# Performance work log

Hardware: AMD Instinct MI355X
Metric: run time of the kernel (lower is better)

## Reference

```python
import jax, jax.numpy as jnp
import numpy as np

T = 1048576      # signal length
K = 3            # number of IMFs
ALPHA = 2000.0   # bandwidth penalty
TAU = 1e-7       # dual ascent step
TOL = 1e-6       # convergence tolerance
N_ITER = 50      # max fixed-point iterations


def _vmd(x, omega_init):
    T_ = x.shape[0]
    t = jnp.arange(1, T_ + 1, dtype=jnp.float32) / T_
    freqs = t - 0.5 - 1.0 / T_                           # [T]
    f_hat = jnp.fft.fftshift(jnp.fft.fft(x))             # [T] complex
    u0 = jnp.zeros((K, T_), dtype=f_hat.dtype)
    lam0 = jnp.zeros((T_,), dtype=f_hat.dtype)

    def step(carry, n):
        u_prev, lam_prev, omega, done = carry
        base = (freqs[None, :] - omega[:, None]) ** 2    # [K,T]
        # mode k's denom also gets (freqs-omega[k-1])^2 and (freqs-omega[k+1])^2
        nbr = jnp.zeros_like(base).at[1:].add(base[:-1]).at[:-1].add(base[1:])
        denom = base + nbr + TAU ** 2
        u_hat = (f_hat[None, :] - lam_prev[None, :] / 2.0) / (1.0 + ALPHA * denom)
        pw = jnp.real(u_hat) ** 2 + jnp.imag(u_hat) ** 2  # |u_hat|^2, [K,T]
        omega_new = jnp.sum(freqs[None, :] * pw, axis=1) / jnp.sum(pw, axis=1)
        lam_new = lam_prev + TAU * (jnp.sum(u_hat, axis=0) - f_hat)
        # convergence check (every 10th iter), mirrors the original break
        u_diff = jnp.sum(jnp.abs(u_hat - u_prev) ** 2) / jnp.sum(jnp.abs(u_prev) ** 2)
        om_diff = jnp.sum(jnp.abs(omega_new - jnp.roll(omega_new, 1))) / K
        conv = (n % 10 == 0) & (u_diff < TOL) & (om_diff < TOL)
        # freeze state once converged (break-iteration's fresh u_hat is kept)
        u_out = jnp.where(done, u_prev, u_hat)
        lam_out = jnp.where(done, lam_prev, lam_new)
        om_out = jnp.where(done, omega, omega_new)
        return (u_out, lam_out, om_out, done | conv), None

    init = (u0, lam0, omega_init.astype(jnp.float32), jnp.array(False))
    (u_hat, _, _, _), _ = jax.lax.scan(jax.checkpoint(step), init, jnp.arange(N_ITER))
    imfs = jnp.real(jnp.fft.ifft(jnp.fft.ifftshift(u_hat, axes=-1), axis=-1))
    return imfs.astype(jnp.float32)                      # [K,T]


def setup_inputs() -> dict:
    key = jax.random.key(0)
    kx, ko = jax.random.split(key)
    x = jax.random.normal(kx, (T,), dtype=jnp.float32)
    omega_init = jax.random.uniform(ko, (K,), dtype=jnp.float32) * 0.5  # init==1
    return {"x": x, "omega_init": omega_init}


def reference(x, omega_init):
    return _vmd(x, omega_init)
```

## Files before the change

### kernel.cpp

```cpp
#include <hip/hip_runtime.h>
#include <math.h>


#define ALPHA_F 2000.0f
#define TAU_F   1e-7f

static __device__ __forceinline__ int lpad2(int i) { return i + (i >> 4); }
static __device__ __forceinline__ int swz(int i)  { return ((i & 7) << 7) | (i >> 3); }
static __device__ __forceinline__ int swzA(int i) { return ((i & 7) << 6) | (i >> 3); }
static __device__ __forceinline__ float frcp(float x) { return __builtin_amdgcn_rcpf(x); }

typedef float v2f __attribute__((ext_vector_type(2)));
static __device__ __forceinline__ v2f sp(float s) { v2f r; r.x = s; r.y = s; return r; }
static __device__ __forceinline__ v2f v2(float a, float b) { v2f r; r.x = a; r.y = b; return r; }
static __device__ __forceinline__ v2f pkfma(v2f a, v2f b, v2f c)
{ return __builtin_elementwise_fma(a, b, c); }
static __device__ __forceinline__ v2f cmul(v2f a, v2f w)
{
  v2f t = a * sp(w.x);
  v2f s = v2(-a.y, a.x);
  return pkfma(s, sp(w.y), t);
}
static __device__ __forceinline__ v2f cmulrr(v2f a, float wr, float wi)
{
  v2f t = a * sp(wr);
  v2f s = v2(-a.y, a.x);
  return pkfma(s, sp(wi), t);
}

#define PADN2 1088

template<int CTRL>
static __device__ __forceinline__ float dpp_addf(float v)
{
  int r = __builtin_amdgcn_update_dpp(0, __float_as_int(v), CTRL, 0xf, 0xf, true);
  return v + __int_as_float(r);
}
static __device__ __forceinline__ float wave64_sum(float v)
{
  v = dpp_addf<0x111>(v);
  v = dpp_addf<0x112>(v);
  v = dpp_addf<0x114>(v);
  v = dpp_addf<0x118>(v);
  v = dpp_addf<0x142>(v);
  v = dpp_addf<0x143>(v);
  return v;
}
static __device__ __forceinline__ float row16_sum(float v)
{
  v = dpp_addf<0x111>(v);
  v = dpp_addf<0x112>(v);
  v = dpp_addf<0x114>(v);
  v = dpp_addf<0x118>(v);
  return v;
}
static __device__ __forceinline__ float rdlane(float v, int l)
{
  return __int_as_float(__builtin_amdgcn_readlane(__float_as_int(v), l));
}

template<int SIGN>
static __device__ void fft1024p_reg(v2f X0, v2f X1, v2f X2, v2f X3,
                                    v2f* A, v2f* B)
{
  const int u = threadIdx.x;
  {
    v2f t0 = X0 + X2, t1 = X0 - X2, t2 = X1 + X3, t3 = X1 - X3;
    v2f o0 = t0 + t2, o2 = t0 - t2;
    v2f ns3 = v2(t3.y, -t3.x);
    v2f o1, o3;
    if (SIGN < 0) { o1 = t1 + ns3; o3 = t1 - ns3; }
    else          { o1 = t1 - ns3; o3 = t1 + ns3; }
    const int base = u << 2;
    B[lpad2(base    )] = o0; B[lpad2(base + 1)] = o1;
    B[lpad2(base + 2)] = o2; B[lpad2(base + 3)] = o3;
    __syncthreads();
  }
#pragma unroll
  for (int st = 1; st < 5; ++st) {
    v2f *in  = (st & 1) ? B : A;
    v2f *out = (st & 1) ? A : B;
    const int quarter = 1 << (2 * st);
    const int p = u & (quarter - 1);
    const int g = u >> (2 * st);

    float sw, cw;
    sincospif((float)(2 * p) * (1.0f / (float)(4 << (2 * st))), &sw, &cw);
    const float w1r = cw, w1i = (SIGN < 0) ? -sw : sw;
    const float w2r = w1r * w1r - w1i * w1i, w2i = 2.0f * w1r * w1i;
    const float w3r = w2r * w1r - w2i * w1i, w3i = w2r * w1i + w2i * w1r;

    v2f Y0 = in[lpad2(u)], Y1 = in[lpad2(u + 256)];
    v2f Y2 = in[lpad2(u + 512)], Y3 = in[lpad2(u + 768)];

    v2f y1 = cmulrr(Y1, w1r, w1i), y2 = cmulrr(Y2, w2r, w2i),
        y3 = cmulrr(Y3, w3r, w3i);

    v2f t0 = Y0 + y2, t1 = Y0 - y2, t2 = y1 + y3, t3 = y1 - y3;
    v2f o0 = t0 + t2, o2 = t0 - t2;
    v2f ns3 = v2(t3.y, -t3.x);
    v2f o1, o3;
    if (SIGN < 0) { o1 = t1 + ns3; o3 = t1 - ns3; }
    else          { o1 = t1 - ns3; o3 = t1 + ns3; }

    const int base = (g << (2 * st + 2)) + p;
    out[lpad2(base              )] = o0;
    out[lpad2(base +     quarter)] = o1;
    out[lpad2(base + 2 * quarter)] = o2;
    out[lpad2(base + 3 * quarter)] = o3;
    __syncthreads();
  }
}

__global__ __launch_bounds__(256) void k_fwd_passA(const float* __restrict__ x,
                                                   float2* __restrict__ ws0)
{
  __shared__ __align__(16) v2f A[PADN2], B[PADN2];
  const int p = swzA(blockIdx.x);
  const int tid = threadIdx.x;
  const int c0 = 2 * p;
  v2f X[4];
#pragma unroll
  for (int q = 0; q < 4; ++q)
    X[q] = ((const v2f*)x)[(size_t)(tid + 256 * q) * 512 + p];
  fft1024p_reg<-1>(X[0], X[1], X[2], X[3], A, B);

  float sa, ca, sb, cb, ssa, cca, ssb, ccb;
  sincospif((float)(c0 * tid) * (2.0f / 1048576.0f), &sa, &ca);
  sincospif((float)((c0 + 1) * tid) * (2.0f / 1048576.0f), &sb, &cb);
  sincospif((float)c0 * (1.0f / 2048.0f), &ssa, &cca);
  sincospif((float)(c0 + 1) * (1.0f / 2048.0f), &ssb, &ccb);
  v2f E0 = v2(ca, -sa), E1 = v2(cb, -sb);
  const v2f S0 = v2(cca, -ssa), S1 = v2(ccb, -ssb);
#pragma unroll
  for (int q = 0; q < 4; ++q) {
    int k = tid + 256 * q;
    int kk = (1024 - k) & 1023;
    v2f Z = B[lpad2(k)];
    v2f Wv = B[lpad2(kk)];
    float X0r = 0.5f * (Z.x + Wv.x), X0i = 0.5f * (Z.y - Wv.y);
    float X1r = 0.5f * (Z.y + Wv.y), X1i = 0.5f * (Wv.x - Z.x);
    v2f o01 = cmul(v2(X0r, X0i), E0);
    v2f o23 = cmul(v2(X1r, X1i), E1);
    float4 o = make_float4(o01.x, o01.y, o23.x, o23.y);
    ((float4*)ws0)[(size_t)k * 512 + p] = o;
    E0 = cmul(E0, S0); E1 = cmul(E1, S1);
  }
}

__global__ __launch_bounds__(256) void k_fwd_passB(const float2* __restrict__ ws0,
                                                   float2* __restrict__ fhat,
                                                   float* __restrict__ ET)
{
  __shared__ __align__(16) v2f A[PADN2], B[PADN2];
  const int b = swz(blockIdx.x);
  const int tid = threadIdx.x;
  v2f X[4];
#pragma unroll
  for (int q = 0; q < 4; ++q)
    X[q] = ((const v2f*)ws0)[(size_t)b * 1024 + tid + 256 * q];
  fft1024p_reg<-1>(X[0], X[1], X[2], X[3], A, B);
#pragma unroll
  for (int q = 0; q < 4; ++q) {
    int k2 = tid + 256 * q;
    v2f v = B[lpad2(k2)];
    fhat[(size_t)b * 1024 + k2] = make_float2(v.x, v.y);
    ET[(size_t)k2 * 1024 + b] = v.x * v.x + v.y * v.y;
  }
}

static __device__ __forceinline__ void lag4(float x, float& l0, float& l1,
                                            float& l2, float& l3)
{
  float m0 = x, m1 = x - (1.0f / 3.0f), m2 = x - (2.0f / 3.0f), m3 = x - 1.0f;
  l0 = -4.5f * m1 * m2 * m3;
  l1 = 13.5f * m0 * m2 * m3;
  l2 = -13.5f * m0 * m1 * m3;
  l3 =  4.5f * m0 * m1 * m2;
}

__global__ __launch_bounds__(256) void k_moments(const float* __restrict__ ET,
                                                 double* __restrict__ W)
{
  __shared__ double red[4 * 4];
  const int B = blockIdx.x;
  const int k2 = B ^ 512;
  const int tid = threadIdx.x;
  double a0 = 0, a1 = 0, a2 = 0, a3 = 0;
#pragma unroll
  for (int q = 0; q < 4; ++q) {
    int k1 = tid + 256 * q;
    float e = ET[(size_t)k2 * 1024 + k1];
    float l0, l1, l2, l3;
    lag4((float)k1 * (1.0f / 1024.0f), l0, l1, l2, l3);
    a0 += (double)(e * l0); a1 += (double)(e * l1);
    a2 += (double)(e * l2); a3 += (double)(e * l3);
  }
  const int lane = tid & 63, wv = tid >> 6;
  double pv[4] = { a0, a1, a2, a3 };
#pragma unroll
  for (int j = 0; j < 4; ++j) {
    double v = pv[j];
    for (int off = 32; off; off >>= 1) v += __shfl_down(v, off, 64);
    if (lane == 0) red[wv * 4 + j] = v;
  }
  __syncthreads();
  if (tid < 4)
    W[B * 4 + tid] = red[tid] + red[4 + tid] + red[8 + tid] + red[12 + tid];
}

__global__ __launch_bounds__(1024) void k_solve(
    const double* __restrict__ W4, const float* __restrict__ omega_init,
    float* __restrict__ ckeepN, float* __restrict__ omegaF)
{
  __shared__ float red[2][6 * 16];
  const int t = threadIdx.x;
  const int lane = t & 63, wv = t >> 6;

  float Wsc[4], fsc[4];
#pragma unroll
  for (int e = 0; e < 4; ++e) {
    Wsc[e] = (float)W4[t * 4 + e];
    fsc[e] = (float)((double)t / 1024.0 + (double)e / 3072.0 - 0.5);
  }
  const v2f frP = v2(fsc[0], fsc[1]), frQ = v2(fsc[2], fsc[3]);
  const v2f WrP = v2(Wsc[0], Wsc[1]), WrQ = v2(Wsc[2], Wsc[3]);
  const v2f WfP = WrP * frP,          WfQ = WrQ * frQ;
  v2f cnrP = sp(0.0f), cnrQ = sp(0.0f);

  float om0 = omega_init[0], om1 = omega_init[1], om2 = omega_init[2];

#pragma unroll 1
  for (int it = 0; it < 49; ++it) {
    float* rb = red[it & 1];
    v2f p0 = sp(0.f), p1 = sp(0.f), p2 = sp(0.f),
        p3 = sp(0.f), p4 = sp(0.f), p5 = sp(0.f);

    auto node_pair = [&](const v2f fv, const v2f Wrv, const v2f Wfv, v2f& cnv) {
      v2f a0 = fv - sp(om0), a1 = fv - sp(om1), a2 = fv - sp(om2);
      v2f d0 = a0 * a0, d1 = a1 * a1, d2 = a2 * a2;
      v2f s01 = d0 + d1, s12 = d1 + d2;
      v2f dA = pkfma(sp(ALPHA_F), s01, sp(1.0f));
      v2f dC = pkfma(sp(ALPHA_F), s12, sp(1.0f));
      v2f dB = pkfma(sp(ALPHA_F), d2, dA);
      v2f AB = dA * dB, BC = dB * dC, AC = dA * dC;
      v2f ABC = AB * dC;
      v2f r = v2(frcp(ABC.x), frcp(ABC.y));
      v2f w0 = BC * r, w1 = AC * r, w2 = AB * r;
      v2f hf = pkfma(sp(-0.5f), cnv, sp(1.0f));
      v2f g = hf * hf;
      v2f gw0 = g * (w0 * w0), gw1 = g * (w1 * w1), gw2 = g * (w2 * w2);
      p0 = pkfma(Wfv, gw0, p0); p1 = pkfma(Wfv, gw1, p1); p2 = pkfma(Wfv, gw2, p2);
      p3 = pkfma(Wrv, gw0, p3); p4 = pkfma(Wrv, gw1, p4); p5 = pkfma(Wrv, gw2, p5);
      v2f S = (w0 + w1) + w2;
      cnv = pkfma(sp(TAU_F), pkfma(S, hf, sp(-1.0f)), cnv);
    };
    node_pair(frP, WrP, WfP, cnrP);
    node_pair(frQ, WrQ, WfQ, cnrQ);

    float q0 = p0.x + p0.y, q1 = p1.x + p1.y, q2 = p2.x + p2.y;
    float q3 = p3.x + p3.y, q4 = p4.x + p4.y, q5 = p5.x + p5.y;

    q0 = wave64_sum(q0); q1 = wave64_sum(q1); q2 = wave64_sum(q2);
    q3 = wave64_sum(q3); q4 = wave64_sum(q4); q5 = wave64_sum(q5);
    if (lane == 63) {
      rb[0 * 16 + wv] = q0; rb[1 * 16 + wv] = q1; rb[2 * 16 + wv] = q2;
      rb[3 * 16 + wv] = q3; rb[4 * 16 + wv] = q4; rb[5 * 16 + wv] = q5;
    }
    __syncthreads();
    float v1 = rb[lane];
    float v2_ = rb[64 + (lane & 31)];
    v1 = row16_sum(v1);
    v2_ = row16_sum(v2_);
    float n0 = rdlane(v1, 15), n1 = rdlane(v1, 31), n2 = rdlane(v1, 47);
    float e0 = rdlane(v1, 63), e1 = rdlane(v2_, 15), e2 = rdlane(v2_, 31);
    om0 = n0 * frcp(e0);
    om1 = n1 * frcp(e1);
    om2 = n2 * frcp(e2);
  }

  ((float4*)ckeepN)[t] = make_float4(cnrP.x, cnrP.y, cnrQ.x, cnrQ.y);
  if (t == 0) { omegaF[0] = om0; omegaF[1] = om1; omegaF[2] = om2; }
}

__global__ __launch_bounds__(256) void k_inv_A2(
    const float2* __restrict__ fhat, const float* __restrict__ ckeepN,
    const float* __restrict__ omegaF, float2* __restrict__ ws0)
{
  __shared__ __align__(16) v2f A[PADN2], B[PADN2];
  __shared__ float cn4[4096];
  __shared__ float som[3];
  const int tid = threadIdx.x;
  const int b = swz(blockIdx.x);
  for (int i = tid; i < 1024; i += 256)
    ((float4*)cn4)[i] = ((const float4*)ckeepN)[i];
  if (tid == 0) { som[0] = omegaF[0]; som[1] = omegaF[1]; som[2] = omegaF[2]; }
  __syncthreads();
  const float om0 = som[0], om1 = som[1], om2 = som[2];
  const float xb = (float)b * (1.0f / 1024.0f);
  float l0, l1, l2, l3, m0, m1, m2, m3;
  lag4(xb, l0, l1, l2, l3);
  lag4(1.0f - xb, m0, m1, m2, m3);

  v2f X[4];
  v2f v2reg[4];
#pragma unroll
  for (int q = 0; q < 4; ++q) {
    int j = tid + 256 * q;
    float2 f = fhat[(size_t)b * 1024 + j];
    int bin = j ^ 512;
    int binp = 1023 - bin;
    float4 cv = ((const float4*)cn4)[bin];
    float4 cw = ((const float4*)cn4)[binp];
    float c  = l0 * cv.x + l1 * cv.y + l2 * cv.z + l3 * cv.w;
    float cp = m0 * cw.x + m1 * cw.y + m2 * cw.z + m3 * cw.w;
    float hf = 1.0f - 0.5f * c;
    float hp = 1.0f - 0.5f * cp;
    int tt = (bin << 10) | b;
    float freq = (float)tt * (1.0f / 1048576.0f) - 0.5f;
    v2f fpm = v2(freq, -freq);
    v2f A0 = fpm - sp(om0), A1 = fpm - sp(om1), A2v = fpm - sp(om2);
    v2f D0 = A0 * A0, D1 = A1 * A1, D2 = A2v * A2v;
    v2f DA = pkfma(sp(ALPHA_F), D0 + D1, sp(1.0f));
    v2f DB = pkfma(sp(ALPHA_F), D2, DA);
    float r0 = hf * frcp(DA.x), r0n = hp * frcp(DA.y);
    float r1 = hf * frcp(DB.x), r1n = hp * frcp(DB.y);
    float Rr = 0.5f * (r0 + r0n), Ri = 0.5f * (r1 + r1n);
    X[q] = cmul(v2(f.x, f.y), v2(Rr, Ri));
    v2f DC = pkfma(sp(ALPHA_F), D1 + D2, sp(1.0f));
    float r2 = hf * frcp(DC.x), r2n = hp * frcp(DC.y);
    float Rr2 = 0.5f * (r2 + r2n);
    v2reg[q] = v2(f.x, f.y) * sp(Rr2);
  }
  fft1024p_reg<1>(X[0], X[1], X[2], X[3], A, B);

  float sa, ca, ss, cs;
  sincospif((float)(b * tid) * (2.0f / 1048576.0f), &sa, &ca);
  sincospif((float)b * (1.0f / 2048.0f), &ss, &cs);
  const v2f Einit = v2(ca, sa);
  const v2f S = v2(cs, ss);

  v2f E = Einit;
#pragma unroll
  for (int q = 0; q < 4; ++q) {
    int m1i = tid + 256 * q;
    v2f v = B[lpad2(m1i)];
    v2f o = cmul(v, E);
    ws0[(size_t)m1i * 1024 + b] = make_float2(o.x, o.y);
    E = cmul(E, S);
  }
  __syncthreads();
  fft1024p_reg<1>(v2reg[0], v2reg[1], v2reg[2], v2reg[3], A, B);

  E = Einit;
#pragma unroll
  for (int q = 0; q < 4; ++q) {
    int m1i = tid + 256 * q;
    v2f v = B[lpad2(m1i)];
    v2f o = cmul(v, E);
    ws0[1048576 + (size_t)m1i * 1024 + b] = make_float2(o.x, o.y);
    E = cmul(E, S);
  }
}

__global__ __launch_bounds__(256) void k_inv_B2(const float2* __restrict__ ws0,
                                                float* __restrict__ out)
{
  __shared__ __align__(16) v2f A[PADN2], B[PADN2];
  const int tid = threadIdx.x;
  const float sc = 1.0f / 1048576.0f;

  if (blockIdx.x < 1024) {
    const int b = swz(blockIdx.x);
    v2f X[4];
#pragma unroll
    for (int q = 0; q < 4; ++q)
      X[q] = ((const v2f*)ws0)[(size_t)b * 1024 + tid + 256 * q];
    fft1024p_reg<1>(X[0], X[1], X[2], X[3], A, B);
#pragma unroll
    for (int q = 0; q < 4; ++q) {
      int m2 = tid + 256 * q;
      v2f v = B[lpad2(m2)];
      out[(size_t)m2 * 1024 + b]           = v.x * sc;
      out[1048576 + (size_t)m2 * 1024 + b] = v.y * sc;
    }
  } else {
    const int s = swzA(blockIdx.x - 1024);
    const int b0 = 2 * s, b1 = 2 * s + 1;
#pragma unroll
    for (int q = 0; q < 4; ++q) {
      int j = tid + 256 * q;
      A[lpad2(j)] = ((const v2f*)ws0)[1048576 + (size_t)b0 * 1024 + j];
      B[lpad2(j)] = ((const v2f*)ws0)[1048576 + (size_t)b1 * 1024 + j];
    }
    __syncthreads();
    v2f Z[4];
#pragma unroll
    for (int q = 0; q < 4; ++q) {
      int j = tid + 256 * q;
      int mj = (1024 - j) & 1023;
      v2f W0j = A[lpad2(j)], W0m = A[lpad2(mj)];
      v2f W1j = B[lpad2(j)], W1m = B[lpad2(mj)];
      float H0r = 0.5f * (W0j.x + W0m.x), H0i = 0.5f * (W0j.y - W0m.y);
      float H1r = 0.5f * (W1j.x + W1m.x), H1i = 0.5f * (W1j.y - W1m.y);
      Z[q] = v2(H0r - H1i, H0i + H1r);
    }
    __syncthreads();
    fft1024p_reg<1>(Z[0], Z[1], Z[2], Z[3], A, B);
#pragma unroll
    for (int q = 0; q < 4; ++q) {
      int m2 = tid + 256 * q;
      v2f v = B[lpad2(m2)];
      out[2097152 + (size_t)m2 * 1024 + b0] = v.x * sc;
      out[2097152 + (size_t)m2 * 1024 + b1] = v.y * sc;
    }
  }
}

extern "C" void kernel_launch(void* const* d_in, const int* in_sizes, int n_in,
                              void* d_out, int out_size, void* d_ws, size_t ws_size,
                              hipStream_t stream)
{
  (void)in_sizes; (void)n_in; (void)out_size; (void)ws_size;
  const float* x       = (const float*)d_in[0];
  const float* om_init = (const float*)d_in[1];
  float* out = (float*)d_out;

  char* w = (char*)d_ws;
  const size_t MB = 1024ull * 1024ull;
  float2* fhat     = (float2*)(w);
  float*  ET       = (float*)(w + 8 * MB);
  double* W4       = (double*)(w + 12 * MB);
  float*  ckeepN   = (float*)(w + 12 * MB + 32 * 1024);
  float*  omegaF   = (float*)(w + 12 * MB + 48 * 1024);
  float2* scratch  = (float2*)(w + 16 * MB);

  k_fwd_passA<<<512, 256, 0, stream>>>(x, scratch);
  k_fwd_passB<<<1024, 256, 0, stream>>>(scratch, fhat, ET);
  k_moments<<<1024, 256, 0, stream>>>(ET, W4);
  k_solve<<<1, 1024, 0, stream>>>(W4, om_init, ckeepN, omegaF);
  k_inv_A2<<<1024, 256, 0, stream>>>(fhat, ckeepN, omegaF, scratch);
  k_inv_B2<<<1536, 256, 0, stream>>>(scratch, out);
}
```

Baseline: 178.8 us.

## Interleave the two inverse FFTs in inv_A2 and halve the solve block

```diff
diff --git a/kernel.cpp b/kernel.cpp
--- a/kernel.cpp
+++ b/kernel.cpp
@@ -46,17 +46,40 @@
   v = dpp_addf<0x143>(v);
   return v;
 }
-static __device__ __forceinline__ float row16_sum(float v)
+static __device__ __forceinline__ float row8_sum(float v)
 {
   v = dpp_addf<0x111>(v);
   v = dpp_addf<0x112>(v);
   v = dpp_addf<0x114>(v);
-  v = dpp_addf<0x118>(v);
   return v;
 }
 static __device__ __forceinline__ float rdlane(float v, int l)
 {
   return __int_as_float(__builtin_amdgcn_readlane(__float_as_int(v), l));
+}
+
+template<int SIGN>
+static __device__ __forceinline__ void bfly4(v2f Y0, v2f Y1, v2f Y2, v2f Y3,
+    float w1r, float w1i, float w2r, float w2i, float w3r, float w3i,
+    v2f& o0, v2f& o1, v2f& o2, v2f& o3)
+{
+  v2f y1 = cmulrr(Y1, w1r, w1i), y2 = cmulrr(Y2, w2r, w2i),
+      y3 = cmulrr(Y3, w3r, w3i);
+  v2f t0 = Y0 + y2, t1 = Y0 - y2, t2 = y1 + y3, t3 = y1 - y3;
+  o0 = t0 + t2; o2 = t0 - t2;
+  v2f ns3 = v2(t3.y, -t3.x);
+  if (SIGN < 0) { o1 = t1 + ns3; o3 = t1 - ns3; }
+  else          { o1 = t1 - ns3; o3 = t1 + ns3; }
+}
+template<int SIGN>
+static __device__ __forceinline__ void bfly4_nt(v2f X0, v2f X1, v2f X2, v2f X3,
+    v2f& o0, v2f& o1, v2f& o2, v2f& o3)
+{
+  v2f t0 = X0 + X2, t1 = X0 - X2, t2 = X1 + X3, t3 = X1 - X3;
+  o0 = t0 + t2; o2 = t0 - t2;
+  v2f ns3 = v2(t3.y, -t3.x);
+  if (SIGN < 0) { o1 = t1 + ns3; o3 = t1 - ns3; }
+  else          { o1 = t1 - ns3; o3 = t1 + ns3; }
 }
 
 template<int SIGN>
@@ -65,12 +88,8 @@
 {
   const int u = threadIdx.x;
   {
-    v2f t0 = X0 + X2, t1 = X0 - X2, t2 = X1 + X3, t3 = X1 - X3;
-    v2f o0 = t0 + t2, o2 = t0 - t2;
-    v2f ns3 = v2(t3.y, -t3.x);
-    v2f o1, o3;
-    if (SIGN < 0) { o1 = t1 + ns3; o3 = t1 - ns3; }
-    else          { o1 = t1 - ns3; o3 = t1 + ns3; }
+    v2f o0, o1, o2, o3;
+    bfly4_nt<SIGN>(X0, X1, X2, X3, o0, o1, o2, o3);
     const int base = u << 2;
     B[lpad2(base    )] = o0; B[lpad2(base + 1)] = o1;
     B[lpad2(base + 2)] = o2; B[lpad2(base + 3)] = o3;
@@ -90,24 +109,67 @@
     const float w2r = w1r * w1r - w1i * w1i, w2i = 2.0f * w1r * w1i;
     const float w3r = w2r * w1r - w2i * w1i, w3i = w2r * w1i + w2i * w1r;
 
-    v2f Y0 = in[lpad2(u)], Y1 = in[lpad2(u + 256)];
-    v2f Y2 = in[lpad2(u + 512)], Y3 = in[lpad2(u + 768)];
-
-    v2f y1 = cmulrr(Y1, w1r, w1i), y2 = cmulrr(Y2, w2r, w2i),
-        y3 = cmulrr(Y3, w3r, w3i);
-
-    v2f t0 = Y0 + y2, t1 = Y0 - y2, t2 = y1 + y3, t3 = y1 - y3;
-    v2f o0 = t0 + t2, o2 = t0 - t2;
-    v2f ns3 = v2(t3.y, -t3.x);
-    v2f o1, o3;
-    if (SIGN < 0) { o1 = t1 + ns3; o3 = t1 - ns3; }
-    else          { o1 = t1 - ns3; o3 = t1 + ns3; }
+    v2f o0, o1, o2, o3;
+    bfly4<SIGN>(in[lpad2(u)], in[lpad2(u + 256)],
+                in[lpad2(u + 512)], in[lpad2(u + 768)],
+                w1r, w1i, w2r, w2i, w3r, w3i, o0, o1, o2, o3);
 
     const int base = (g << (2 * st + 2)) + p;
     out[lpad2(base              )] = o0;
     out[lpad2(base +     quarter)] = o1;
     out[lpad2(base + 2 * quarter)] = o2;
     out[lpad2(base + 3 * quarter)] = o3;
+    __syncthreads();
+  }
+}
+
+template<int SIGN>
+static __device__ void fft1024p_dual(const v2f X[4], const v2f Y[4],
+                                     v2f* A1, v2f* B1, v2f* A2, v2f* B2)
+{
+  const int u = threadIdx.x;
+  {
+    v2f o0, o1, o2, o3, p0, p1, p2, p3;
+    bfly4_nt<SIGN>(X[0], X[1], X[2], X[3], o0, o1, o2, o3);
+    bfly4_nt<SIGN>(Y[0], Y[1], Y[2], Y[3], p0, p1, p2, p3);
+    const int base = u << 2;
+    B1[lpad2(base    )] = o0; B1[lpad2(base + 1)] = o1;
+    B1[lpad2(base + 2)] = o2; B1[lpad2(base + 3)] = o3;
+    B2[lpad2(base    )] = p0; B2[lpad2(base + 1)] = p1;
+    B2[lpad2(base + 2)] = p2; B2[lpad2(base + 3)] = p3;
+    __syncthreads();
+  }
+#pragma unroll
+  for (int st = 1; st < 5; ++st) {
+    v2f *in1  = (st & 1) ? B1 : A1, *out1 = (st & 1) ? A1 : B1;
+    v2f *in2  = (st & 1) ? B2 : A2, *out2 = (st & 1) ? A2 : B2;
+    const int quarter = 1 << (2 * st);
+    const int p = u & (quarter - 1);
+    const int g = u >> (2 * st);
+
+    float sw, cw;
+    sincospif((float)(2 * p) * (1.0f / (float)(4 << (2 * st))), &sw, &cw);
+    const float w1r = cw, w1i = (SIGN < 0) ? -sw : sw;
+    const float w2r = w1r * w1r - w1i * w1i, w2i = 2.0f * w1r * w1i;
+    const float w3r = w2r * w1r - w2i * w1i, w3i = w2r * w1i + w2i * w1r;
+
+    v2f o0, o1, o2, o3, p0, p1, p2, p3;
+    bfly4<SIGN>(in1[lpad2(u)], in1[lpad2(u + 256)],
+                in1[lpad2(u + 512)], in1[lpad2(u + 768)],
+                w1r, w1i, w2r, w2i, w3r, w3i, o0, o1, o2, o3);
+    bfly4<SIGN>(in2[lpad2(u)], in2[lpad2(u + 256)],
+                in2[lpad2(u + 512)], in2[lpad2(u + 768)],
+                w1r, w1i, w2r, w2i, w3r, w3i, p0, p1, p2, p3);
+
+    const int base = (g << (2 * st + 2)) + p;
+    out1[lpad2(base              )] = o0;
+    out1[lpad2(base +     quarter)] = o1;
+    out1[lpad2(base + 2 * quarter)] = o2;
+    out1[lpad2(base + 3 * quarter)] = o3;
+    out2[lpad2(base              )] = p0;
+    out2[lpad2(base +     quarter)] = p1;
+    out2[lpad2(base + 2 * quarter)] = p2;
+    out2[lpad2(base + 3 * quarter)] = p3;
     __syncthreads();
   }
 }
@@ -209,25 +271,29 @@
     W[B * 4 + tid] = red[tid] + red[4 + tid] + red[8 + tid] + red[12 + tid];
 }
 
-__global__ __launch_bounds__(1024) void k_solve(
+__global__ __launch_bounds__(512) void k_solve(
     const double* __restrict__ W4, const float* __restrict__ omega_init,
     float* __restrict__ ckeepN, float* __restrict__ omegaF)
 {
-  __shared__ float red[2][6 * 16];
+  __shared__ float red[2][64];
   const int t = threadIdx.x;
   const int lane = t & 63, wv = t >> 6;
 
-  float Wsc[4], fsc[4];
-#pragma unroll
-  for (int e = 0; e < 4; ++e) {
-    Wsc[e] = (float)W4[t * 4 + e];
-    fsc[e] = (float)((double)t / 1024.0 + (double)e / 3072.0 - 0.5);
-  }
-  const v2f frP = v2(fsc[0], fsc[1]), frQ = v2(fsc[2], fsc[3]);
-  const v2f WrP = v2(Wsc[0], Wsc[1]), WrQ = v2(Wsc[2], Wsc[3]);
-  const v2f WfP = WrP * frP,          WfQ = WrQ * frQ;
-  v2f cnrP = sp(0.0f), cnrQ = sp(0.0f);
-
+  float Wsc[8], fsc[8];
+#pragma unroll
+  for (int e = 0; e < 8; ++e) {
+    Wsc[e] = (float)W4[t * 8 + e];
+    int bin = 2 * t + (e >> 2);
+    fsc[e] = (float)((double)bin / 1024.0 + (double)(e & 3) / 3072.0 - 0.5);
+  }
+  v2f frA[4], WrA[4], WfA[4], cnA[4];
+#pragma unroll
+  for (int i = 0; i < 4; ++i) {
+    frA[i] = v2(fsc[2 * i], fsc[2 * i + 1]);
+    WrA[i] = v2(Wsc[2 * i], Wsc[2 * i + 1]);
+    WfA[i] = WrA[i] * frA[i];
+    cnA[i] = sp(0.0f);
+  }
   float om0 = omega_init[0], om1 = omega_init[1], om2 = omega_init[2];
 
 #pragma unroll 1
@@ -236,7 +302,9 @@
     v2f p0 = sp(0.f), p1 = sp(0.f), p2 = sp(0.f),
         p3 = sp(0.f), p4 = sp(0.f), p5 = sp(0.f);
 
-    auto node_pair = [&](const v2f fv, const v2f Wrv, const v2f Wfv, v2f& cnv) {
+#pragma unroll
+    for (int i = 0; i < 4; ++i) {
+      const v2f fv = frA[i];
       v2f a0 = fv - sp(om0), a1 = fv - sp(om1), a2 = fv - sp(om2);
       v2f d0 = a0 * a0, d1 = a1 * a1, d2 = a2 * a2;
       v2f s01 = d0 + d1, s12 = d1 + d2;
@@ -245,18 +313,19 @@
       v2f dB = pkfma(sp(ALPHA_F), d2, dA);
       v2f AB = dA * dB, BC = dB * dC, AC = dA * dC;
       v2f ABC = AB * dC;
-      v2f r = v2(frcp(ABC.x), frcp(ABC.y));
+      float rr = frcp(ABC.x * ABC.y);
+      v2f r = v2(rr * ABC.y, rr * ABC.x);
       v2f w0 = BC * r, w1 = AC * r, w2 = AB * r;
-      v2f hf = pkfma(sp(-0.5f), cnv, sp(1.0f));
+      v2f hf = pkfma(sp(-0.5f), cnA[i], sp(1.0f));
       v2f g = hf * hf;
       v2f gw0 = g * (w0 * w0), gw1 = g * (w1 * w1), gw2 = g * (w2 * w2);
-      p0 = pkfma(Wfv, gw0, p0); p1 = pkfma(Wfv, gw1, p1); p2 = pkfma(Wfv, gw2, p2);
-      p3 = pkfma(Wrv, gw0, p3); p4 = pkfma(Wrv, gw1, p4); p5 = pkfma(Wrv, gw2, p5);
+      p0 = pkfma(WfA[i], gw0, p0); p1 = pkfma(WfA[i], gw1, p1);
+      p2 = pkfma(WfA[i], gw2, p2);
+      p3 = pkfma(WrA[i], gw0, p3); p4 = pkfma(WrA[i], gw1, p4);
+      p5 = pkfma(WrA[i], gw2, p5);
       v2f S = (w0 + w1) + w2;
-      cnv = pkfma(sp(TAU_F), pkfma(S, hf, sp(-1.0f)), cnv);
-    };
-    node_pair(frP, WrP, WfP, cnrP);
-    node_pair(frQ, WrQ, WfQ, cnrQ);
+      cnA[i] = pkfma(sp(TAU_F), pkfma(S, hf, sp(-1.0f)), cnA[i]);
+    }
 
     float q0 = p0.x + p0.y, q1 = p1.x + p1.y, q2 = p2.x + p2.y;
     float q3 = p3.x + p3.y, q4 = p4.x + p4.y, q5 = p5.x + p5.y;
@@ -264,22 +333,21 @@
     q0 = wave64_sum(q0); q1 = wave64_sum(q1); q2 = wave64_sum(q2);
     q3 = wave64_sum(q3); q4 = wave64_sum(q4); q5 = wave64_sum(q5);
     if (lane == 63) {
-      rb[0 * 16 + wv] = q0; rb[1 * 16 + wv] = q1; rb[2 * 16 + wv] = q2;
-      rb[3 * 16 + wv] = q3; rb[4 * 16 + wv] = q4; rb[5 * 16 + wv] = q5;
+      rb[0 * 8 + wv] = q0; rb[1 * 8 + wv] = q1; rb[2 * 8 + wv] = q2;
+      rb[3 * 8 + wv] = q3; rb[4 * 8 + wv] = q4; rb[5 * 8 + wv] = q5;
     }
     __syncthreads();
     float v1 = rb[lane];
-    float v2_ = rb[64 + (lane & 31)];
-    v1 = row16_sum(v1);
-    v2_ = row16_sum(v2_);
-    float n0 = rdlane(v1, 15), n1 = rdlane(v1, 31), n2 = rdlane(v1, 47);
-    float e0 = rdlane(v1, 63), e1 = rdlane(v2_, 15), e2 = rdlane(v2_, 31);
+    v1 = row8_sum(v1);
+    float n0 = rdlane(v1, 7),  n1 = rdlane(v1, 15), n2 = rdlane(v1, 23);
+    float e0 = rdlane(v1, 31), e1 = rdlane(v1, 39), e2 = rdlane(v1, 47);
     om0 = n0 * frcp(e0);
     om1 = n1 * frcp(e1);
     om2 = n2 * frcp(e2);
   }
 
-  ((float4*)ckeepN)[t] = make_float4(cnrP.x, cnrP.y, cnrQ.x, cnrQ.y);
+  ((float4*)ckeepN)[2 * t]     = make_float4(cnA[0].x, cnA[0].y, cnA[1].x, cnA[1].y);
+  ((float4*)ckeepN)[2 * t + 1] = make_float4(cnA[2].x, cnA[2].y, cnA[3].x, cnA[3].y);
   if (t == 0) { omegaF[0] = om0; omegaF[1] = om1; omegaF[2] = om2; }
 }
 
@@ -287,31 +355,26 @@
     const float2* __restrict__ fhat, const float* __restrict__ ckeepN,
     const float* __restrict__ omegaF, float2* __restrict__ ws0)
 {
-  __shared__ __align__(16) v2f A[PADN2], B[PADN2];
-  __shared__ float cn4[4096];
-  __shared__ float som[3];
+  __shared__ __align__(16) v2f A1[PADN2], B1[PADN2], A2[PADN2], B2[PADN2];
   const int tid = threadIdx.x;
   const int b = swz(blockIdx.x);
-  for (int i = tid; i < 1024; i += 256)
-    ((float4*)cn4)[i] = ((const float4*)ckeepN)[i];
-  if (tid == 0) { som[0] = omegaF[0]; som[1] = omegaF[1]; som[2] = omegaF[2]; }
-  __syncthreads();
-  const float om0 = som[0], om1 = som[1], om2 = som[2];
+  const float om0 = omegaF[0], om1 = omegaF[1], om2 = omegaF[2];
   const float xb = (float)b * (1.0f / 1024.0f);
   float l0, l1, l2, l3, m0, m1, m2, m3;
   lag4(xb, l0, l1, l2, l3);
   lag4(1.0f - xb, m0, m1, m2, m3);
+  const float4* cN = (const float4*)ckeepN;
 
   v2f X[4];
-  v2f v2reg[4];
+  v2f Y[4];
 #pragma unroll
   for (int q = 0; q < 4; ++q) {
     int j = tid + 256 * q;
     float2 f = fhat[(size_t)b * 1024 + j];
     int bin = j ^ 512;
     int binp = 1023 - bin;
-    float4 cv = ((const float4*)cn4)[bin];
-    float4 cw = ((const float4*)cn4)[binp];
+    float4 cv = cN[bin];
+    float4 cw = cN[binp];
     float c  = l0 * cv.x + l1 * cv.y + l2 * cv.z + l3 * cv.w;
     float cp = m0 * cw.x + m1 * cw.y + m2 * cw.z + m3 * cw.w;
     float hf = 1.0f - 0.5f * c;
@@ -319,8 +382,8 @@
     int tt = (bin << 10) | b;
     float freq = (float)tt * (1.0f / 1048576.0f) - 0.5f;
     v2f fpm = v2(freq, -freq);
-    v2f A0 = fpm - sp(om0), A1 = fpm - sp(om1), A2v = fpm - sp(om2);
-    v2f D0 = A0 * A0, D1 = A1 * A1, D2 = A2v * A2v;
+    v2f A0 = fpm - sp(om0), A1v = fpm - sp(om1), A2v = fpm - sp(om2);
+    v2f D0 = A0 * A0, D1 = A1v * A1v, D2 = A2v * A2v;
     v2f DA = pkfma(sp(ALPHA_F), D0 + D1, sp(1.0f));
     v2f DB = pkfma(sp(ALPHA_F), D2, DA);
     float r0 = hf * frcp(DA.x), r0n = hp * frcp(DA.y);
@@ -330,35 +393,24 @@
     v2f DC = pkfma(sp(ALPHA_F), D1 + D2, sp(1.0f));
     float r2 = hf * frcp(DC.x), r2n = hp * frcp(DC.y);
     float Rr2 = 0.5f * (r2 + r2n);
-    v2reg[q] = v2(f.x, f.y) * sp(Rr2);
-  }
-  fft1024p_reg<1>(X[0], X[1], X[2], X[3], A, B);
+    Y[q] = v2(f.x, f.y) * sp(Rr2);
+  }
+  fft1024p_dual<1>(X, Y, A1, B1, A2, B2);
 
   float sa, ca, ss, cs;
   sincospif((float)(b * tid) * (2.0f / 1048576.0f), &sa, &ca);
   sincospif((float)b * (1.0f / 2048.0f), &ss, &cs);
-  const v2f Einit = v2(ca, sa);
+  v2f E = v2(ca, sa);
   const v2f S = v2(cs, ss);
-
-  v2f E = Einit;
 #pragma unroll
   for (int q = 0; q < 4; ++q) {
     int m1i = tid + 256 * q;
-    v2f v = B[lpad2(m1i)];
-    v2f o = cmul(v, E);
-    ws0[(size_t)m1i * 1024 + b] = make_float2(o.x, o.y);
-    E = cmul(E, S);
-  }
-  __syncthreads();
-  fft1024p_reg<1>(v2reg[0], v2reg[1], v2reg[2], v2reg[3], A, B);
-
-  E = Einit;
-#pragma unroll
-  for (int q = 0; q < 4; ++q) {
-    int m1i = tid + 256 * q;
-    v2f v = B[lpad2(m1i)];
-    v2f o = cmul(v, E);
-    ws0[1048576 + (size_t)m1i * 1024 + b] = make_float2(o.x, o.y);
+    v2f va = B1[lpad2(m1i)];
+    v2f vb = B2[lpad2(m1i)];
+    v2f oa = cmul(va, E);
+    v2f ob = cmul(vb, E);
+    ws0[(size_t)m1i * 1024 + b]           = make_float2(oa.x, oa.y);
+    ws0[1048576 + (size_t)m1i * 1024 + b] = make_float2(ob.x, ob.y);
     E = cmul(E, S);
   }
 }
@@ -438,7 +490,7 @@
   k_fwd_passA<<<512, 256, 0, stream>>>(x, scratch);
   k_fwd_passB<<<1024, 256, 0, stream>>>(scratch, fhat, ET);
   k_moments<<<1024, 256, 0, stream>>>(ET, W4);
-  k_solve<<<1, 1024, 0, stream>>>(W4, om_init, ckeepN, omegaF);
+  k_solve<<<1, 512, 0, stream>>>(W4, om_init, ckeepN, omegaF);
   k_inv_A2<<<1024, 256, 0, stream>>>(fhat, ckeepN, omegaF, scratch);
   k_inv_B2<<<1536, 256, 0, stream>>>(scratch, out);
 }
```

Measured after the change: 170.3 us. 1.05x faster.
